# Optimization experiments

Hardware: AMD Instinct MI355X
Metric: run time of the kernel (lower is better)

The kernel has to match this reference:

```python
import jax, jax.numpy as jnp
import numpy as np

N_NODES = 100000
N_EDGES = 600000
HIDDEN = 128


def setup_inputs() -> dict:
    key = jax.random.key(0)
    ks = jax.random.split(key, 5)
    x = jax.random.normal(ks[0], (N_NODES, HIDDEN), dtype=jnp.float32)
    edge_index = jax.random.randint(ks[1], (2, N_EDGES), 0, N_NODES, dtype=jnp.int64)
    edge_weight = jax.random.uniform(ks[2], (N_EDGES,), dtype=jnp.float32)
    # MLP params: Linear(2*H+1 -> H), ReLU, Linear(H -> 1)
    W1 = jax.random.normal(ks[3], (2 * HIDDEN + 1, HIDDEN), dtype=jnp.float32) * (1.0 / np.sqrt(2 * HIDDEN + 1))
    b1 = jnp.zeros((HIDDEN,), dtype=jnp.float32)
    W2 = jax.random.normal(ks[4], (HIDDEN, 1), dtype=jnp.float32) * (1.0 / np.sqrt(HIDDEN))
    b2 = jnp.zeros((1,), dtype=jnp.float32)
    return {"x": x, "edge_index": edge_index, "edge_weight": edge_weight,
            "W1": W1, "b1": b1, "W2": W2, "b2": b2}


def reference(x, edge_index, edge_weight, W1, b1, W2, b2):
    num_nodes = x.shape[0]
    src = edge_index[0]
    tgt = edge_index[1]
    h_src = x[src]                      # [E, H] gather
    h_tgt = x[tgt]                      # [E, H] gather
    w = edge_weight[:, None]            # [E, 1]
    concat = jnp.concatenate([h_src, h_tgt, w], axis=-1)   # [E, 2H+1]
    hidden = jax.nn.relu(concat @ W1 + b1)                 # [E, H]
    scores = (hidden @ W2 + b2)[:, 0]                      # [E]
    # NOTE: the original _softmax_edge's max-pass uses index_put_(accumulate=True)
    # on a -inf buffer, so every touched entry stays -inf and is then replaced by 0;
    # the net effect is NO max subtraction. Faithful math: plain exp / segment_sum.
    exp_scores = jnp.exp(scores)
    sum_exp = jax.ops.segment_sum(exp_scores, tgt, num_segments=num_nodes)
    sum_exp = jnp.maximum(sum_exp, 1e-12)
    alpha = exp_scores / sum_exp[tgt]                      # [E]
    out = jax.ops.segment_sum(alpha[:, None] * h_src, tgt, num_segments=num_nodes)
    return x + out
```

## Files before the change

### kernel.cpp

```cpp
#include <hip/hip_runtime.h>
#include <hip/hip_bf16.h>

#define N_NODES 100000
#define N_EDGES 600000
#define HID 128
#define SCAN_NB 391
#define GEMM_BLOCKS 1563
#define COUNT_BLOCKS 586


typedef short bf16x8 __attribute__((ext_vector_type(8)));
typedef float f32x4  __attribute__((ext_vector_type(4)));

__device__ inline unsigned short f2bf(float v) {
    __hip_bfloat16 h = __float2bfloat16(v);
    return *(unsigned short*)&h;
}
__device__ inline unsigned int pack2(float a, float b) {
    return (unsigned int)f2bf(a) | ((unsigned int)f2bf(b) << 16);
}
__device__ inline float2 bfpair(unsigned int u) {
    float lo = __uint_as_float(u << 16);
    float hi = __uint_as_float(u & 0xffff0000u);
    return make_float2(lo, hi);
}
__device__ inline void lds_barrier() {
    asm volatile("s_waitcnt lgkmcnt(0)" ::: "memory");
    __builtin_amdgcn_s_barrier();
}

__global__ __launch_bounds__(256) void k_prepW1(const float* __restrict__ W1,
                                                unsigned short* __restrict__ Bh)
{
    int idx = blockIdx.x * 256 + threadIdx.x;
    int n = idx & 255;
    int k = idx >> 8;
    float v = (n < HID) ? W1[k * HID + n] : W1[(HID + k) * HID + (n - HID)];
    Bh[(k >> 5) * 8192 + n * 32 + (k & 31)] = f2bf(v);
}

__global__ __launch_bounds__(256) void k_gemm_count(const float* __restrict__ x,
                                                    const unsigned short* __restrict__ BhG,
                                                    unsigned short* __restrict__ zbuf,
                                                    unsigned short* __restrict__ y2buf,
                                                    const int* __restrict__ ei,
                                                    int* __restrict__ deg,
                                                    int* __restrict__ rank)
{
    __shared__ unsigned short Ah[64 * 128];

    if (blockIdx.x >= GEMM_BLOCKS) {
        int cb = blockIdx.x - GEMM_BLOCKS;
        for (int e = cb * 256 + threadIdx.x; e < N_EDGES; e += COUNT_BLOCKS * 256) {
            rank[e] = atomicAdd(&deg[ei[N_EDGES + e]], 1);
        }
        return;
    }

    const int tid  = threadIdx.x;
    const int bm   = blockIdx.x * 64;
    const int wave = tid >> 6;
    const int lane = tid & 63;
    const int q    = lane >> 4;
    const int ln   = lane & 15;

    {
        const int r  = tid >> 2;
        const int c  = tid & 3;
        const int gm = bm + r;
        const bool ok = gm < N_NODES;
        const float* px = &x[(size_t)gm * HID + c * 32];

        float4 v0 = make_float4(0.f,0.f,0.f,0.f), v1=v0, v2=v0, v3=v0, v4=v0, v5=v0, v6=v0, v7=v0;
        if (ok) {
            v0 = *(const float4*)(px + 0);  v1 = *(const float4*)(px + 4);
            v2 = *(const float4*)(px + 8);  v3 = *(const float4*)(px + 12);
            v4 = *(const float4*)(px + 16); v5 = *(const float4*)(px + 20);
            v6 = *(const float4*)(px + 24); v7 = *(const float4*)(px + 28);
        }
        uint4 ch0, ch1, ch2, ch3;
        ch0.x = pack2(v0.x, v0.y); ch0.y = pack2(v0.z, v0.w); ch0.z = pack2(v1.x, v1.y); ch0.w = pack2(v1.z, v1.w);
        ch1.x = pack2(v2.x, v2.y); ch1.y = pack2(v2.z, v2.w); ch1.z = pack2(v3.x, v3.y); ch1.w = pack2(v3.z, v3.w);
        ch2.x = pack2(v4.x, v4.y); ch2.y = pack2(v4.z, v4.w); ch2.z = pack2(v5.x, v5.y); ch2.w = pack2(v5.z, v5.w);
        ch3.x = pack2(v6.x, v6.y); ch3.y = pack2(v6.z, v6.w); ch3.z = pack2(v7.x, v7.y); ch3.w = pack2(v7.z, v7.w);

        char* rowp = (char*)Ah + r * 256;
        const int swz = (r & 7) << 4;
        *(uint4*)(rowp + ((c * 64 +  0) ^ swz)) = ch0;
        *(uint4*)(rowp + ((c * 64 + 16) ^ swz)) = ch1;
        *(uint4*)(rowp + ((c * 64 + 32) ^ swz)) = ch2;
        *(uint4*)(rowp + ((c * 64 + 48) ^ swz)) = ch3;

        if (ok) {
            unsigned short* zp = &zbuf[(size_t)gm * 256 + 128 + c * 32];
            *(uint4*)(zp + 0)  = ch0;
            *(uint4*)(zp + 8)  = ch1;
            *(uint4*)(zp + 16) = ch2;
            *(uint4*)(zp + 24) = ch3;
        }
    }
    lds_barrier();

    bf16x8 ah[4][4];
    {
        const int swzr = (ln & 7) << 4;
        #pragma unroll
        for (int mt = 0; mt < 4; ++mt) {
            const char* rowp = (const char*)Ah + (mt * 16 + ln) * 256;
            #pragma unroll
            for (int ks = 0; ks < 4; ++ks) {
                ah[mt][ks] = *(const bf16x8*)(rowp + ((ks * 64 + q * 16) ^ swzr));
            }
        }
    }

    f32x4 acc[4][4] = {};
    #pragma unroll
    for (int nt = 0; nt < 4; ++nt) {
        bf16x8 bh[4];
        #pragma unroll
        for (int ks = 0; ks < 4; ++ks) {
            bh[ks] = *(const bf16x8*)&BhG[ks * 8192 + (wave * 64 + nt * 16 + ln) * 32 + q * 8];
        }
        #pragma unroll
        for (int mt = 0; mt < 4; ++mt) {
            #pragma unroll
            for (int ks = 0; ks < 4; ++ks) {
                acc[mt][nt] = __builtin_amdgcn_mfma_f32_16x16x32_bf16(bh[ks], ah[mt][ks], acc[mt][nt], 0, 0, 0);
            }
        }
    }

    #pragma unroll
    for (int mt = 0; mt < 4; ++mt) {
        int node = bm + mt * 16 + ln;
        if (node < N_NODES) {
            #pragma unroll
            for (int nt = 0; nt < 4; ++nt) {
                int col0 = wave * 64 + nt * 16 + q * 4;
                unsigned int lo = pack2(acc[mt][nt][0], acc[mt][nt][1]);
                unsigned int hi = pack2(acc[mt][nt][2], acc[mt][nt][3]);
                if (col0 < 128) *(uint2*)&zbuf[(size_t)node * 256 + col0] = make_uint2(lo, hi);
                else            *(uint2*)&y2buf[(size_t)node * 128 + (col0 - 128)] = make_uint2(lo, hi);
            }
        }
    }
}

__global__ __launch_bounds__(256) void k_rowptr(const int* __restrict__ deg,
                                                int* __restrict__ rowptr)
{
    __shared__ int s[256];
    int t = threadIdx.x;
    int b = blockIdx.x;
    int lim = b * 256;

    int acc = 0;
    for (int i = t; i < lim; i += 256) acc += deg[i];
    s[t] = acc;
    __syncthreads();
    #pragma unroll
    for (int off = 128; off > 0; off >>= 1) {
        if (t < off) s[t] += s[t + off];
        __syncthreads();
    }
    int pb = s[0];
    __syncthreads();

    int idx = lim + t;
    int v = (idx < N_NODES) ? deg[idx] : 0;
    s[t] = v;
    __syncthreads();
    #pragma unroll
    for (int off = 1; off < 256; off <<= 1) {
        int u = (t >= off) ? s[t - off] : 0;
        __syncthreads();
        s[t] += u;
        __syncthreads();
    }
    if (idx < N_NODES) rowptr[idx] = pb + s[t] - v;
    if (idx == 0) rowptr[N_NODES] = N_EDGES;
}

__global__ __launch_bounds__(256) void k_fill(const int* __restrict__ ei,
                                              const float* __restrict__ ew,
                                              const int* __restrict__ rowptr,
                                              const int* __restrict__ rank,
                                              uint2* __restrict__ eprs)
{
    for (int e = blockIdx.x * 256 + threadIdx.x; e < N_EDGES; e += COUNT_BLOCKS * 256) {
        int tgt = ei[N_EDGES + e];
        int pos = rowptr[tgt] + rank[e];
        eprs[pos] = make_uint2((unsigned int)ei[e], __float_as_uint(ew[e]));
    }
}

__global__ __launch_bounds__(256) void k_fused(const unsigned int* __restrict__ zu,
                                               const unsigned int* __restrict__ y2u,
                                               const int* __restrict__ rowptr,
                                               const uint2* __restrict__ eprs,
                                               const float* __restrict__ x,
                                               const float* __restrict__ W1,
                                               const float* __restrict__ b1,
                                               const float* __restrict__ W2,
                                               const float* __restrict__ b2,
                                               float* __restrict__ out)
{
    int n = (blockIdx.x * blockDim.x + threadIdx.x) >> 6;
    int lane = threadIdx.x & 63;
    if (n >= N_NODES) return;
    int ql = lane & 15;
    int qi = lane >> 4;
    int c0 = ql * 8;

    uint4 uy2 = *(const uint4*)&y2u[(size_t)n * 64 + ql * 4];
    float2 y2a = bfpair(uy2.x), y2b = bfpair(uy2.y), y2c = bfpair(uy2.z), y2d = bfpair(uy2.w);
    float4 bv0 = *(const float4*)&b1[c0];
    float4 bv1 = *(const float4*)&b1[c0 + 4];
    float4 wr0 = *(const float4*)&W1[256 * HID + c0];
    float4 wr1 = *(const float4*)&W1[256 * HID + c0 + 4];
    float4 w20 = *(const float4*)&W2[c0];
    float4 w21 = *(const float4*)&W2[c0 + 4];
    float p0 = y2a.x + bv0.x, p1 = y2a.y + bv0.y, p2 = y2b.x + bv0.z, p3 = y2b.y + bv0.w;
    float p4 = y2c.x + bv1.x, p5 = y2c.y + bv1.y, p6 = y2d.x + bv1.z, p7 = y2d.y + bv1.w;
    float b2v = b2[0];

    int beg = rowptr[n], end = rowptr[n + 1];
    float a0 = 0.f, a1 = 0.f, a2 = 0.f, a3 = 0.f;
    float a4 = 0.f, a5 = 0.f, a6 = 0.f, a7 = 0.f;
    float denom = 0.f;

    for (int i = beg; i < end; i += 4) {
        int idx = i + qi;
        bool valid = idx < end;
        int ie = valid ? idx : (end - 1);
        uint2 ep = eprs[ie];
        size_t base = (size_t)ep.x * 128;
        float w = __uint_as_float(ep.y);
        uint4 uy = *(const uint4*)&zu[base + ql * 4];
        uint4 ux = *(const uint4*)&zu[base + 64 + ql * 4];

        float2 ya = bfpair(uy.x), yb = bfpair(uy.y), yc = bfpair(uy.z), yd = bfpair(uy.w);
        float h0 = fmaxf(fmaf(w, wr0.x, ya.x + p0), 0.f);
        float h1 = fmaxf(fmaf(w, wr0.y, ya.y + p1), 0.f);
        float h2 = fmaxf(fmaf(w, wr0.z, yb.x + p2), 0.f);
        float h3 = fmaxf(fmaf(w, wr0.w, yb.y + p3), 0.f);
        float h4 = fmaxf(fmaf(w, wr1.x, yc.x + p4), 0.f);
        float h5 = fmaxf(fmaf(w, wr1.y, yc.y + p5), 0.f);
        float h6 = fmaxf(fmaf(w, wr1.z, yd.x + p6), 0.f);
        float h7 = fmaxf(fmaf(w, wr1.w, yd.y + p7), 0.f);
        float s = ((h0 * w20.x + h1 * w20.y) + (h2 * w20.z + h3 * w20.w))
                + ((h4 * w21.x + h5 * w21.y) + (h6 * w21.z + h7 * w21.w));
        #pragma unroll
        for (int m = 1; m <= 8; m <<= 1) s += __shfl_xor(s, m, 64);
        float es = valid ? __expf(s + b2v) : 0.f;

        float2 xa = bfpair(ux.x), xb = bfpair(ux.y), xc = bfpair(ux.z), xd = bfpair(ux.w);
        a0 = fmaf(es, xa.x, a0); a1 = fmaf(es, xa.y, a1);
        a2 = fmaf(es, xb.x, a2); a3 = fmaf(es, xb.y, a3);
        a4 = fmaf(es, xc.x, a4); a5 = fmaf(es, xc.y, a5);
        a6 = fmaf(es, xd.x, a6); a7 = fmaf(es, xd.y, a7);
        denom += es;
    }

    #pragma unroll
    for (int m = 16; m <= 32; m <<= 1) {
        a0 += __shfl_xor(a0, m, 64); a1 += __shfl_xor(a1, m, 64);
        a2 += __shfl_xor(a2, m, 64); a3 += __shfl_xor(a3, m, 64);
        a4 += __shfl_xor(a4, m, 64); a5 += __shfl_xor(a5, m, 64);
        a6 += __shfl_xor(a6, m, 64); a7 += __shfl_xor(a7, m, 64);
        denom += __shfl_xor(denom, m, 64);
    }

    if (qi == 0) {
        float4 xt0 = *(const float4*)&x[(size_t)n * HID + c0];
        float4 xt1 = *(const float4*)&x[(size_t)n * HID + c0 + 4];
        float inv = 1.0f / fmaxf(denom, 1e-12f);
        float4 o0, o1;
        o0.x = xt0.x + a0 * inv; o0.y = xt0.y + a1 * inv;
        o0.z = xt0.z + a2 * inv; o0.w = xt0.w + a3 * inv;
        o1.x = xt1.x + a4 * inv; o1.y = xt1.y + a5 * inv;
        o1.z = xt1.z + a6 * inv; o1.w = xt1.w + a7 * inv;
        *(float4*)&out[(size_t)n * HID + c0]     = o0;
        *(float4*)&out[(size_t)n * HID + c0 + 4] = o1;
    }
}

extern "C" void kernel_launch(void* const* d_in, const int* in_sizes, int n_in,
                              void* d_out, int out_size, void* d_ws, size_t ws_size,
                              hipStream_t stream) {
    const float* x  = (const float*)d_in[0];
    const int*   ei = (const int*)d_in[1];
    const float* ew = (const float*)d_in[2];
    const float* W1 = (const float*)d_in[3];
    const float* b1 = (const float*)d_in[4];
    const float* W2 = (const float*)d_in[5];
    const float* b2 = (const float*)d_in[6];
    float* out = (float*)d_out;
    char* ws = (char*)d_ws;

    const size_t deg_b    = 400000;
    const size_t rowptr_b = 400016;
    const size_t rank_b   = 2400000;
    const size_t eprs_b   = 4800000;
    const size_t Bh_b     = 65536;

    char* p = ws;
    int* deg      = (int*)p;             p += deg_b;
    int* rowptr   = (int*)p;             p += rowptr_b;
    int* rank     = (int*)p;             p += rank_b;
    uint2* eprs   = (uint2*)p;           p += eprs_b;
    unsigned short* BhG = (unsigned short*)p;  p += Bh_b;
    unsigned short* zbuf  = (unsigned short*)p;  p += (size_t)N_NODES * 256 * 2;
    unsigned short* y2buf = (unsigned short*)p;

    const int node_wave_blocks = (N_NODES * 64 + 255) / 256;

    hipMemsetAsync(deg, 0, 400000, stream);
    hipLaunchKernelGGL(k_prepW1, dim3(128), dim3(256), 0, stream, W1, BhG);
    hipLaunchKernelGGL(k_gemm_count, dim3(GEMM_BLOCKS + COUNT_BLOCKS), dim3(256), 0, stream,
                       x, BhG, zbuf, y2buf, ei, deg, rank);
    hipLaunchKernelGGL(k_rowptr, dim3(SCAN_NB), dim3(256), 0, stream, deg, rowptr);
    hipLaunchKernelGGL(k_fill,   dim3(COUNT_BLOCKS), dim3(256), 0, stream, ei, ew, rowptr, rank, eprs);
    hipLaunchKernelGGL(k_fused,  dim3(node_wave_blocks), dim3(256), 0, stream,
                       (const unsigned int*)zbuf, (const unsigned int*)y2buf,
                       rowptr, eprs, x, W1, b1, W2, b2, out);
}
```

Baseline: 301.2 us.

## Regroup kernels: fuse W1 prep with degree count, overlap GEMM with CSR fill

The W1 bf16 repack now runs in the same launch as the per-edge degree counting, and the node GEMM now runs alongside the CSR fill instead of alongside the counting. This cuts one kernel launch and moves the GEMM so it can overlap the fill phase rather than delaying the scan. Counting now uses one thread per edge across 2344 blocks instead of a grid-stride loop. The launch order still keeps the scan after counting and the fill after the scan.

Result: no change. 304.3 us (+1.0%).

```diff
diff --git a/kernel.cpp b/kernel.cpp
--- a/kernel.cpp
+++ b/kernel.cpp
@@ -6,7 +6,9 @@
 #define HID 128
 #define SCAN_NB 391
 #define GEMM_BLOCKS 1563
-#define COUNT_BLOCKS 586
+#define FILL_BLOCKS 586
+#define PREP_BLOCKS 128
+#define COUNT_BLOCKS 2344
 
 
 typedef short bf16x8 __attribute__((ext_vector_type(8)));
@@ -29,30 +31,77 @@
     __builtin_amdgcn_s_barrier();
 }
 
-__global__ __launch_bounds__(256) void k_prepW1(const float* __restrict__ W1,
-                                                unsigned short* __restrict__ Bh)
-{
-    int idx = blockIdx.x * 256 + threadIdx.x;
-    int n = idx & 255;
-    int k = idx >> 8;
-    float v = (n < HID) ? W1[k * HID + n] : W1[(HID + k) * HID + (n - HID)];
-    Bh[(k >> 5) * 8192 + n * 32 + (k & 31)] = f2bf(v);
-}
-
-__global__ __launch_bounds__(256) void k_gemm_count(const float* __restrict__ x,
-                                                    const unsigned short* __restrict__ BhG,
-                                                    unsigned short* __restrict__ zbuf,
-                                                    unsigned short* __restrict__ y2buf,
+__global__ __launch_bounds__(256) void k_prep_count(const float* __restrict__ W1,
+                                                    unsigned short* __restrict__ Bh,
                                                     const int* __restrict__ ei,
                                                     int* __restrict__ deg,
                                                     int* __restrict__ rank)
 {
+    if (blockIdx.x < PREP_BLOCKS) {
+        int idx = blockIdx.x * 256 + threadIdx.x;
+        int n = idx & 255;
+        int k = idx >> 8;
+        float v = (n < HID) ? W1[k * HID + n] : W1[(HID + k) * HID + (n - HID)];
+        Bh[(k >> 5) * 8192 + n * 32 + (k & 31)] = f2bf(v);
+        return;
+    }
+    int e = (blockIdx.x - PREP_BLOCKS) * 256 + threadIdx.x;
+    if (e < N_EDGES) rank[e] = atomicAdd(&deg[ei[N_EDGES + e]], 1);
+}
+
+__global__ __launch_bounds__(256) void k_rowptr(const int* __restrict__ deg,
+                                                int* __restrict__ rowptr)
+{
+    __shared__ int s[256];
+    int t = threadIdx.x;
+    int b = blockIdx.x;
+    int lim = b * 256;
+
+    int acc = 0;
+    for (int i = t; i < lim; i += 256) acc += deg[i];
+    s[t] = acc;
+    __syncthreads();
+    #pragma unroll
+    for (int off = 128; off > 0; off >>= 1) {
+        if (t < off) s[t] += s[t + off];
+        __syncthreads();
+    }
+    int pb = s[0];
+    __syncthreads();
+
+    int idx = lim + t;
+    int v = (idx < N_NODES) ? deg[idx] : 0;
+    s[t] = v;
+    __syncthreads();
+    #pragma unroll
+    for (int off = 1; off < 256; off <<= 1) {
+        int u = (t >= off) ? s[t - off] : 0;
+        __syncthreads();
+        s[t] += u;
+        __syncthreads();
+    }
+    if (idx < N_NODES) rowptr[idx] = pb + s[t] - v;
+    if (idx == 0) rowptr[N_NODES] = N_EDGES;
+}
+
+__global__ __launch_bounds__(256) void k_gemm_fill(const float* __restrict__ x,
+                                                   const unsigned short* __restrict__ BhG,
+                                                   unsigned short* __restrict__ zbuf,
+                                                   unsigned short* __restrict__ y2buf,
+                                                   const int* __restrict__ ei,
+                                                   const float* __restrict__ ew,
+                                                   const int* __restrict__ rowptr,
+                                                   const int* __restrict__ rank,
+                                                   uint2* __restrict__ eprs)
+{
     __shared__ unsigned short Ah[64 * 128];
 
     if (blockIdx.x >= GEMM_BLOCKS) {
-        int cb = blockIdx.x - GEMM_BLOCKS;
-        for (int e = cb * 256 + threadIdx.x; e < N_EDGES; e += COUNT_BLOCKS * 256) {
-            rank[e] = atomicAdd(&deg[ei[N_EDGES + e]], 1);
+        int fb = blockIdx.x - GEMM_BLOCKS;
+        for (int e = fb * 256 + threadIdx.x; e < N_EDGES; e += FILL_BLOCKS * 256) {
+            int tgt = ei[N_EDGES + e];
+            int pos = rowptr[tgt] + rank[e];
+            eprs[pos] = make_uint2((unsigned int)ei[e], __float_as_uint(ew[e]));
         }
         return;
     }
@@ -144,54 +193,6 @@
                 else            *(uint2*)&y2buf[(size_t)node * 128 + (col0 - 128)] = make_uint2(lo, hi);
             }
         }
-    }
-}
-
-__global__ __launch_bounds__(256) void k_rowptr(const int* __restrict__ deg,
-                                                int* __restrict__ rowptr)
-{
-    __shared__ int s[256];
-    int t = threadIdx.x;
-    int b = blockIdx.x;
-    int lim = b * 256;
-
-    int acc = 0;
-    for (int i = t; i < lim; i += 256) acc += deg[i];
-    s[t] = acc;
-    __syncthreads();
-    #pragma unroll
-    for (int off = 128; off > 0; off >>= 1) {
-        if (t < off) s[t] += s[t + off];
-        __syncthreads();
-    }
-    int pb = s[0];
-    __syncthreads();
-
-    int idx = lim + t;
-    int v = (idx < N_NODES) ? deg[idx] : 0;
-    s[t] = v;
-    __syncthreads();
-    #pragma unroll
-    for (int off = 1; off < 256; off <<= 1) {
-        int u = (t >= off) ? s[t - off] : 0;
-        __syncthreads();
-        s[t] += u;
-        __syncthreads();
-    }
-    if (idx < N_NODES) rowptr[idx] = pb + s[t] - v;
-    if (idx == 0) rowptr[N_NODES] = N_EDGES;
-}
-
-__global__ __launch_bounds__(256) void k_fill(const int* __restrict__ ei,
-                                              const float* __restrict__ ew,
-                                              const int* __restrict__ rowptr,
-                                              const int* __restrict__ rank,
-                                              uint2* __restrict__ eprs)
-{
-    for (int e = blockIdx.x * 256 + threadIdx.x; e < N_EDGES; e += COUNT_BLOCKS * 256) {
-        int tgt = ei[N_EDGES + e];
-        int pos = rowptr[tgt] + rank[e];
-        eprs[pos] = make_uint2((unsigned int)ei[e], __float_as_uint(ew[e]));
     }
 }
 
@@ -317,11 +318,11 @@
     const int node_wave_blocks = (N_NODES * 64 + 255) / 256;
 
     hipMemsetAsync(deg, 0, 400000, stream);
-    hipLaunchKernelGGL(k_prepW1, dim3(128), dim3(256), 0, stream, W1, BhG);
-    hipLaunchKernelGGL(k_gemm_count, dim3(GEMM_BLOCKS + COUNT_BLOCKS), dim3(256), 0, stream,
-                       x, BhG, zbuf, y2buf, ei, deg, rank);
+    hipLaunchKernelGGL(k_prep_count, dim3(PREP_BLOCKS + COUNT_BLOCKS), dim3(256), 0, stream,
+                       W1, BhG, ei, deg, rank);
     hipLaunchKernelGGL(k_rowptr, dim3(SCAN_NB), dim3(256), 0, stream, deg, rowptr);
-    hipLaunchKernelGGL(k_fill,   dim3(COUNT_BLOCKS), dim3(256), 0, stream, ei, ew, rowptr, rank, eprs);
+    hipLaunchKernelGGL(k_gemm_fill, dim3(GEMM_BLOCKS + FILL_BLOCKS), dim3(256), 0, stream,
+                       x, BhG, zbuf, y2buf, ei, ew, rowptr, rank, eprs);
     hipLaunchKernelGGL(k_fused,  dim3(node_wave_blocks), dim3(256), 0, stream,
                        (const unsigned int*)zbuf, (const unsigned int*)y2buf,
                        rowptr, eprs, x, W1, b1, W2, b2, out);
```
